# Performance work log

Hardware: AMD Instinct MI355X
Metric: run time of the kernel (lower is better)

The kernel has to match this reference:

```python
import jax, jax.numpy as jnp
import numpy as np

FP8_MAX = 448.0  # finfo(float8_e4m3fn).max
BLK = 128        # block_size = [128, 128]


def _quant_dequant_act(x):
    """Dynamic per-token, per-128-block fp8 quantization followed by dequant.
    Matches fp8_act_quant: scale = amax(block)/448, q = fp8(x/scale), deq = q*scale."""
    T, K = x.shape
    xb = x.reshape(T, K // BLK, BLK)
    amax = jnp.max(jnp.abs(xb), axis=-1, keepdims=True)
    scale = jnp.maximum(amax, 1e-12) / FP8_MAX  # [T, K//BLK, 1]
    q = (xb / scale).astype(jnp.float8_e4m3fn).astype(jnp.float32)
    return (q * scale).reshape(T, K)


def _dequant_weight(w, s):
    """Block-wise dequant of an fp8-valued [N, K] weight with [N//BLK, K//BLK] scales."""
    N, K = w.shape
    wb = w.reshape(N // BLK, BLK, K // BLK, BLK)
    return (wb * s[:, None, :, None]).reshape(N, K)


def setup_inputs() -> dict:
    key = jax.random.key(0)
    ks = jax.random.split(key, 7)
    T, H, I, E, TOPK = 8192, 2048, 1024, 32, 8
    f8 = lambda x: x.astype(jnp.float8_e4m3fn).astype(jnp.float32)  # store fp8-valued weights as f32
    hidden_states = jax.random.normal(ks[0], (T, H), jnp.float32)
    gate_up_proj = f8(jax.random.normal(ks[1], (E, 2 * I, H), jnp.float32))
    gate_up_proj_scale_inv = jax.random.uniform(ks[2], (E, (2 * I) // BLK, H // BLK), jnp.float32, 0.005, 0.02)
    down_proj = f8(jax.random.normal(ks[3], (E, H, I), jnp.float32))
    down_proj_scale_inv = jax.random.uniform(ks[4], (E, H // BLK, I // BLK), jnp.float32, 0.005, 0.02)
    top_k_index = jax.random.randint(ks[5], (T, TOPK), 0, E, jnp.int32)
    tw = jax.random.uniform(ks[6], (T, TOPK), jnp.float32)
    top_k_weights = tw / jnp.sum(tw, axis=-1, keepdims=True)
    return {
        'hidden_states': hidden_states,
        'gate_up_proj': gate_up_proj,
        'gate_up_proj_scale_inv': gate_up_proj_scale_inv,
        'down_proj': down_proj,
        'down_proj_scale_inv': down_proj_scale_inv,
        'top_k_weights': top_k_weights,
        'top_k_index': top_k_index,
    }


def reference(hidden_states, gate_up_proj, gate_up_proj_scale_inv, down_proj,
              down_proj_scale_inv, top_k_weights, top_k_index):
    E = gate_up_proj.shape[0]
    # Dynamic activation quantization is per-token (expert-independent): do it once.
    x_deq = _quant_dequant_act(hidden_states)  # [T, H]
    # Per-expert combine weight: cw[e, t] = sum_k top_k_weights[t,k] * (top_k_index[t,k]==e)
    hit = top_k_index[None, :, :] == jnp.arange(E, dtype=top_k_index.dtype)[:, None, None]
    cw = jnp.sum(jnp.where(hit, top_k_weights[None, :, :], 0.0), axis=-1)  # [E, T]

    def body(acc, xs):
        wgu, sgu, wd, sd, w_tok = xs
        h = x_deq @ _dequant_weight(wgu, sgu).T          # [T, 2I] fp8 grouped GEMM
        gate, up = jnp.split(h, 2, axis=-1)
        h = jax.nn.silu(gate) * up                        # _apply_gate
        h = _quant_dequant_act(h)                         # re-quantize before down_proj
        y = h @ _dequant_weight(wd, sd).T                 # [T, H]
        return acc + w_tok[:, None] * y, None

    acc0 = jnp.zeros_like(hidden_states, dtype=jnp.float32)
    out, _ = jax.lax.scan(
        body, acc0,
        (gate_up_proj, gate_up_proj_scale_inv, down_proj, down_proj_scale_inv, cw))
    return out
```

## Files before the change

kernel.cpp:

```cpp
#include <hip/hip_runtime.h>

typedef float f32x4 __attribute__((ext_vector_type(4)));
typedef float f32x16 __attribute__((ext_vector_type(16)));
typedef _Float16 f16x4 __attribute__((ext_vector_type(4)));
typedef long long i64t;

constexpr int T = 8192, H = 2048, II = 1024, E = 32, TOPK = 8;
constexpr int NSLOT = T * TOPK;
constexpr int MT_MAX = 32;
constexpr int MT1 = 64;

__device__ __forceinline__ i64t frag8(const unsigned char* lds, int row, int kbyte) {
  int c8 = (kbyte >> 3) ^ ((row & 7) << 1) ^ ((row >> 3) & 1);
  return *(const i64t*)(lds + row * 128 + c8 * 8);
}
__device__ __forceinline__ void wr16c(unsigned char* lds, int r, int c, uint4 v) {
  if ((r >> 3) & 1) v = make_uint4(v.z, v.w, v.x, v.y);
  *(uint4*)(lds + r * 128 + ((c ^ (r & 7)) << 4)) = v;
}

__global__ void k_quant_x(const float* __restrict__ x, unsigned char* __restrict__ x8,
                          float* __restrict__ xs) {
  int gw = blockIdx.x * 4 + (threadIdx.x >> 6);
  int lane = threadIdx.x & 63;
  int token = gw >> 4, kb = gw & 15;
  float2 v = *(const float2*)(x + (size_t)token * H + kb * 128 + lane * 2);
  float am = fmaxf(fabsf(v.x), fabsf(v.y));
#pragma unroll
  for (int m = 1; m <= 32; m <<= 1) am = fmaxf(am, __shfl_xor(am, m, 64));
  float scale = fmaxf(am, 1e-12f) / 448.0f;
  int pk = __builtin_amdgcn_cvt_pk_fp8_f32(v.x / scale, v.y / scale, 0, false);
  *(unsigned short*)(x8 + (size_t)token * H + kb * 128 + lane * 2) = (unsigned short)(pk & 0xffff);
  if (lane == 0) xs[token * 16 + kb] = scale;
}

__global__ void k_cvt_w(const float* __restrict__ w, unsigned char* __restrict__ w8, int n4) {
  int i = blockIdx.x * 256 + threadIdx.x;
  if (i >= n4) return;
  f32x4 v = *(const f32x4*)(w + (size_t)i * 4);
  int p = __builtin_amdgcn_cvt_pk_fp8_f32(v[0], v[1], 0, false);
  p = __builtin_amdgcn_cvt_pk_fp8_f32(v[2], v[3], p, true);
  *(unsigned int*)(w8 + (size_t)i * 4) = (unsigned int)p;
}

__global__ void k_count(const int* __restrict__ tki, int* __restrict__ counts) {
  int i = blockIdx.x * 256 + threadIdx.x;
  if (i < NSLOT) atomicAdd(&counts[tki[i]], 1);
}
__global__ void k_scan(const int* __restrict__ counts, int* __restrict__ offsets) {
  if (threadIdx.x == 0) {
    int s = 0;
    for (int e = 0; e < E; ++e) { offsets[e] = s; s += counts[e]; }
    offsets[E] = s;
  }
}
__global__ void k_fill(const int* __restrict__ tki, const float* __restrict__ tkw,
                       const int* __restrict__ offsets, int* __restrict__ cursor,
                       int* __restrict__ tok_list, float* __restrict__ cw_list,
                       int* __restrict__ islot) {
  int i = blockIdx.x * 256 + threadIdx.x;
  if (i < NSLOT) {
    int e = tki[i];
    int pos = atomicAdd(&cursor[e], 1);
    int slot = offsets[e] + pos;
    tok_list[slot] = i >> 3;
    cw_list[slot] = tkw[i];
    islot[i] = slot;
  }
}

__launch_bounds__(256, 2)
__global__ void k_gemm1(const unsigned char* __restrict__ x8, const float* __restrict__ xs,
                        const unsigned char* __restrict__ wgu8, const float* __restrict__ sgu,
                        const int* __restrict__ offsets, const int* __restrict__ tok_list,
                        unsigned char* __restrict__ a8, float* __restrict__ ascale) {
  __shared__ __align__(16) unsigned char lA[64 * 128];
  __shared__ __align__(16) unsigned char lBg[128 * 128];
  __shared__ __align__(16) unsigned char lBu[128 * 128];
  __shared__ float lsx[16 * 64];
  __shared__ int ltok[64];
  __shared__ float lamax[64 * 2];
  __shared__ float lscale[64];

  int bx = blockIdx.x;
  int e = bx >> 9, mt = (bx >> 3) & 63, nt = bx & 7;
  int off0 = offsets[e];
  int Me = offsets[e + 1] - off0;
  if (mt * 64 >= Me) return;
  int vrows = Me - mt * 64; if (vrows > 64) vrows = 64;
  int tid = threadIdx.x;

  if (tid < 64) ltok[tid] = (tid < vrows) ? tok_list[off0 + mt * 64 + tid] : -1;
  __syncthreads();

  if (tid < 128) {
    int r = tid >> 1, h = tid & 1;
    int tokr = ltok[r]; int tk = tokr < 0 ? 0 : tokr;
#pragma unroll
    for (int i = 0; i < 2; ++i) {
      f32x4 v = *(const f32x4*)(xs + (size_t)tk * 16 + h * 8 + i * 4);
#pragma unroll
      for (int j = 0; j < 4; ++j) lsx[(h * 8 + i * 4 + j) * 64 + r] = (tokr < 0) ? 0.0f : v[j];
    }
  }

  const int lane = tid & 63, wid = tid >> 6;
  const int wm = wid >> 1, wn = wid & 1;
  const int l31 = lane & 31, lg = lane >> 5;

  const int ra = tid >> 2, qa = tid & 3;
  const int rb = tid >> 1, hb = tid & 1;
  int tokA = ltok[ra] < 0 ? 0 : ltok[ra];
  const unsigned char* gA = x8 + (size_t)tokA * H + qa * 32;
  const unsigned char* gG = wgu8 + ((size_t)e * 2048 + nt * 128 + rb) * H + hb * 64;
  const unsigned char* gU = gG + (size_t)1024 * H;

  {
    uint4 a0 = *(const uint4*)gA, a1 = *(const uint4*)(gA + 16);
    uint4 g0 = *(const uint4*)gG, g1 = *(const uint4*)(gG + 16);
    uint4 g2 = *(const uint4*)(gG + 32), g3 = *(const uint4*)(gG + 48);
    uint4 u0 = *(const uint4*)gU, u1 = *(const uint4*)(gU + 16);
    uint4 u2 = *(const uint4*)(gU + 32), u3 = *(const uint4*)(gU + 48);
    wr16c(lA, ra, qa * 2 + 0, a0); wr16c(lA, ra, qa * 2 + 1, a1);
    wr16c(lBg, rb, hb * 4 + 0, g0); wr16c(lBg, rb, hb * 4 + 1, g1);
    wr16c(lBg, rb, hb * 4 + 2, g2); wr16c(lBg, rb, hb * 4 + 3, g3);
    wr16c(lBu, rb, hb * 4 + 0, u0); wr16c(lBu, rb, hb * 4 + 1, u1);
    wr16c(lBu, rb, hb * 4 + 2, u2); wr16c(lBu, rb, hb * 4 + 3, u3);
  }
  __syncthreads();

  f32x16 aG[2] = {};
  f32x16 aU[2] = {};

  for (int kb = 0; kb < 16; ++kb) {
    uint4 pA0, pA1, pG0, pG1, pG2, pG3, pU0, pU1, pU2, pU3;
    if (kb < 15) {
      pA0 = *(const uint4*)(gA + (kb + 1) * 128);
      pA1 = *(const uint4*)(gA + (kb + 1) * 128 + 16);
      pG0 = *(const uint4*)(gG + (kb + 1) * 128);
      pG1 = *(const uint4*)(gG + (kb + 1) * 128 + 16);
      pG2 = *(const uint4*)(gG + (kb + 1) * 128 + 32);
      pG3 = *(const uint4*)(gG + (kb + 1) * 128 + 48);
      pU0 = *(const uint4*)(gU + (kb + 1) * 128);
      pU1 = *(const uint4*)(gU + (kb + 1) * 128 + 16);
      pU2 = *(const uint4*)(gU + (kb + 1) * 128 + 32);
      pU3 = *(const uint4*)(gU + (kb + 1) * 128 + 48);
    }

    float swg = sgu[(e * 16 + nt) * 16 + kb];
    float swu = sgu[(e * 16 + 8 + nt) * 16 + kb];

    i64t af[8];
#pragma unroll
    for (int ks = 0; ks < 8; ++ks)
      af[ks] = frag8(lA, wm * 32 + l31, ks * 16 + lg * 8);
    f32x4 sxv[4];
#pragma unroll
    for (int jj = 0; jj < 4; ++jj)
      sxv[jj] = *(const f32x4*)(&lsx[kb * 64 + wm * 32 + jj * 8 + lg * 4]);

#pragma unroll
    for (int gu = 0; gu < 2; ++gu) {
      const unsigned char* lB = gu ? lBu : lBg;
      float sw = gu ? swu : swg;
#pragma unroll
      for (int nf = 0; nf < 2; ++nf) {
        i64t bf[8];
#pragma unroll
        for (int ks = 0; ks < 8; ++ks)
          bf[ks] = frag8(lB, wn * 64 + nf * 32 + l31, ks * 16 + lg * 8);
        f32x16 t = {};
#pragma unroll
        for (int ks = 0; ks < 8; ++ks)
          t = __builtin_amdgcn_mfma_f32_32x32x16_fp8_fp8(af[ks], bf[ks], t, 0, 0, 0);
#pragma unroll
        for (int j = 0; j < 16; ++j) {
          float f = sxv[j >> 2][j & 3] * sw;
          if (gu) aU[nf][j] += t[j] * f; else aG[nf][j] += t[j] * f;
        }
      }
    }

    if (kb < 15) {
      __syncthreads();
      wr16c(lA, ra, qa * 2 + 0, pA0); wr16c(lA, ra, qa * 2 + 1, pA1);
      wr16c(lBg, rb, hb * 4 + 0, pG0); wr16c(lBg, rb, hb * 4 + 1, pG1);
      wr16c(lBg, rb, hb * 4 + 2, pG2); wr16c(lBg, rb, hb * 4 + 3, pG3);
      wr16c(lBu, rb, hb * 4 + 0, pU0); wr16c(lBu, rb, hb * 4 + 1, pU1);
      wr16c(lBu, rb, hb * 4 + 2, pU2); wr16c(lBu, rb, hb * 4 + 3, pU3);
      __syncthreads();
    }
  }

#pragma unroll
  for (int nf = 0; nf < 2; ++nf)
#pragma unroll
    for (int j = 0; j < 16; ++j) {
      float g = aG[nf][j], u = aU[nf][j];
      aG[nf][j] = g * (1.0f / (1.0f + expf(-g))) * u;
    }

#pragma unroll
  for (int j = 0; j < 16; ++j) {
    float m = fmaxf(fabsf(aG[0][j]), fabsf(aG[1][j]));
#pragma unroll
    for (int msk = 1; msk <= 16; msk <<= 1) m = fmaxf(m, __shfl_xor(m, msk, 64));
    if (l31 == 0)
      lamax[(wm * 32 + (j & 3) + ((j >> 2) * 8) + lg * 4) * 2 + wn] = m;
  }
  __syncthreads();
  if (tid < 64) {
    float mm = fmaxf(lamax[tid * 2], lamax[tid * 2 + 1]);
    lscale[tid] = fmaxf(mm, 1e-12f) / 448.0f;
  }
  __syncthreads();

#pragma unroll
  for (int j = 0; j < 16; ++j) {
    int row = wm * 32 + (j & 3) + ((j >> 2) * 8) + lg * 4;
    float sc = lscale[row];
#pragma unroll
    for (int nf = 0; nf < 2; ++nf) {
      int pk = __builtin_amdgcn_cvt_pk_fp8_f32(aG[nf][j] / sc, 0.0f, 0, false);
      lA[row * 128 + wn * 64 + nf * 32 + l31] = (unsigned char)(pk & 0xff);
    }
    if (row < vrows && l31 == 0 && wn == 0)
      ascale[(off0 + mt * 64 + row) * 8 + nt] = sc;
  }
  __syncthreads();
#pragma unroll
  for (int it = 0; it < 2; ++it) {
    int idx = it * 256 + tid;
    int row = idx >> 3, c = idx & 7;
    if (row < vrows)
      *(uint4*)(a8 + (size_t)(off0 + mt * 64 + row) * 1024 + nt * 128 + c * 16) =
          *(const uint4*)(lA + row * 128 + c * 16);
  }
}

__launch_bounds__(256, 2)
__global__ void k_gemm2(const unsigned char* __restrict__ a8, const float* __restrict__ ascale,
                        const unsigned char* __restrict__ wd8, const float* __restrict__ sd,
                        const int* __restrict__ offsets, const float* __restrict__ cw_list,
                        int ntbase, _Float16* __restrict__ yslot) {
  __shared__ __align__(16) unsigned char lbuf[2][2][128 * 128];
  __shared__ float las[8 * 128];
  __shared__ float lcw[128];

  int bx = blockIdx.x;
  int e = bx >> 8, mt = (bx >> 3) & 31, nth = bx & 7;
  int nt = ntbase + nth;
  int off0 = offsets[e];
  int Me = offsets[e + 1] - off0;
  if (mt * 128 >= Me) return;
  int vrows = Me - mt * 128; if (vrows > 128) vrows = 128;
  int tid = threadIdx.x;

  if (tid < 128) lcw[tid] = (tid < vrows) ? cw_list[off0 + mt * 128 + tid] : 0.0f;
  int r = tid >> 1, h = tid & 1;
  int srow = off0 + mt * 128 + r; if (srow > NSLOT - 1) srow = NSLOT - 1;
  {
    f32x4 v = *(const f32x4*)(ascale + (size_t)srow * 8 + h * 4);
#pragma unroll
    for (int j = 0; j < 4; ++j) las[(h * 4 + j) * 128 + r] = v[j];
  }

  const int lane = tid & 63, wid = tid >> 6;
  const int wm = wid >> 1, wn = wid & 1;
  const int l31 = lane & 31, lg = lane >> 5;

  const unsigned char* gA = a8 + (size_t)srow * 1024 + h * 64;
  const unsigned char* gB = wd8 + ((size_t)e * 2048 + nt * 128 + r) * 1024 + h * 64;

  uint4 rA[4], rB[4];
#pragma unroll
  for (int i = 0; i < 4; ++i) { rA[i] = ((const uint4*)gA)[i]; rB[i] = ((const uint4*)gB)[i]; }
#pragma unroll
  for (int i = 0; i < 4; ++i) { wr16c(lbuf[0][0], r, h * 4 + i, rA[i]); wr16c(lbuf[0][1], r, h * 4 + i, rB[i]); }
  __syncthreads();

  f32x16 acc[2][2] = {};
  int cur = 0;

  for (int kb = 0; kb < 8; ++kb) {
    if (kb < 7) {
#pragma unroll
      for (int i = 0; i < 4; ++i) {
        rA[i] = ((const uint4*)(gA + (kb + 1) * 128))[i];
        rB[i] = ((const uint4*)(gB + (kb + 1) * 128))[i];
      }
    }
    const unsigned char* cA = lbuf[cur][0];
    const unsigned char* cB = lbuf[cur][1];
    float swd = sd[(e * 16 + nt) * 8 + kb];
    i64t bf[2][8];
#pragma unroll
    for (int nf = 0; nf < 2; ++nf)
#pragma unroll
      for (int ks = 0; ks < 8; ++ks)
        bf[nf][ks] = frag8(cB, wn * 64 + nf * 32 + l31, ks * 16 + lg * 8);
#pragma unroll
    for (int mf = 0; mf < 2; ++mf) {
      i64t af[8];
#pragma unroll
      for (int ks = 0; ks < 8; ++ks)
        af[ks] = frag8(cA, wm * 64 + mf * 32 + l31, ks * 16 + lg * 8);
      f32x4 sav[4];
#pragma unroll
      for (int jj = 0; jj < 4; ++jj)
        sav[jj] = *(const f32x4*)(&las[kb * 128 + wm * 64 + mf * 32 + jj * 8 + lg * 4]);
#pragma unroll
      for (int nf = 0; nf < 2; ++nf) {
        f32x16 t = {};
#pragma unroll
        for (int ks = 0; ks < 8; ++ks)
          t = __builtin_amdgcn_mfma_f32_32x32x16_fp8_fp8(af[ks], bf[nf][ks], t, 0, 0, 0);
#pragma unroll
        for (int j = 0; j < 16; ++j)
          acc[mf][nf][j] += t[j] * (sav[j >> 2][j & 3] * swd);
      }
    }
    if (kb < 7) {
      unsigned char* nA = lbuf[cur ^ 1][0];
      unsigned char* nB = lbuf[cur ^ 1][1];
#pragma unroll
      for (int i = 0; i < 4; ++i) { wr16c(nA, r, h * 4 + i, rA[i]); wr16c(nB, r, h * 4 + i, rB[i]); }
      __syncthreads();
      cur ^= 1;
    }
  }

  __syncthreads();
  _Float16* lh = (_Float16*)lbuf;
#pragma unroll
  for (int mf = 0; mf < 2; ++mf)
#pragma unroll
    for (int j = 0; j < 16; ++j) {
      int row = wm * 64 + mf * 32 + (j & 3) + ((j >> 2) * 8) + lg * 4;
      float w = lcw[row];
#pragma unroll
      for (int nf = 0; nf < 2; ++nf)
        lh[row * 128 + wn * 64 + nf * 32 + l31] = (_Float16)(acc[mf][nf][j] * w);
    }
  __syncthreads();
#pragma unroll
  for (int it = 0; it < 8; ++it) {
    int idx = it * 256 + tid;
    int row = idx >> 4, u = idx & 15;
    if (row < vrows)
      *(uint4*)((char*)yslot + ((size_t)(off0 + mt * 128 + row) * 1024 + nth * 128) * 2 + u * 16) =
          *(const uint4*)((const char*)lh + row * 256 + u * 16);
  }
}

__global__ void k_reduce(const _Float16* __restrict__ yslot, const int* __restrict__ islot,
                         float* __restrict__ out, int half) {
  __shared__ int ls[8];
  int t = blockIdx.x;
  if (threadIdx.x < 8) ls[threadIdx.x] = islot[t * 8 + threadIdx.x];
  __syncthreads();
  int c = threadIdx.x * 4;
  float s0 = 0, s1 = 0, s2 = 0, s3 = 0;
#pragma unroll
  for (int k = 0; k < 8; ++k) {
    f16x4 v = *(const f16x4*)(yslot + (size_t)ls[k] * 1024 + c);
    s0 += (float)v[0]; s1 += (float)v[1]; s2 += (float)v[2]; s3 += (float)v[3];
  }
  f32x4 r = {s0, s1, s2, s3};
  *(f32x4*)(out + (size_t)t * 2048 + half * 1024 + c) = r;
}

extern "C" void kernel_launch(void* const* d_in, const int* in_sizes, int n_in,
                              void* d_out, int out_size, void* d_ws, size_t ws_size,
                              hipStream_t stream) {
  const float* x   = (const float*)d_in[0];
  const float* wgu = (const float*)d_in[1];
  const float* sgu = (const float*)d_in[2];
  const float* wd  = (const float*)d_in[3];
  const float* sd  = (const float*)d_in[4];
  const float* tkw = (const float*)d_in[5];
  const int*   tki = (const int*)d_in[6];
  float* out = (float*)d_out;

  char* ws = (char*)d_ws;
  size_t o = 0;
  auto alloc = [&](size_t sz) { void* p = ws + o; o = (o + sz + 255) & ~(size_t)255; return p; };
  unsigned char* x8    = (unsigned char*)alloc((size_t)T * H);
  unsigned char* wgu8  = (unsigned char*)alloc((size_t)E * 2 * II * H);
  unsigned char* wd8   = (unsigned char*)alloc((size_t)E * H * II);
  unsigned char* a8    = (unsigned char*)alloc((size_t)NSLOT * II);
  float* xs            = (float*)alloc((size_t)T * 16 * 4);
  float* as_           = (float*)alloc((size_t)NSLOT * 8 * 4);
  int* counts          = (int*)alloc(128);
  int* cursor          = (int*)alloc(128);
  int* offsets         = (int*)alloc(256);
  int* tok_list        = (int*)alloc((size_t)NSLOT * 4);
  float* cw_list       = (float*)alloc((size_t)NSLOT * 4);
  int* islot           = (int*)alloc((size_t)NSLOT * 4);
  _Float16* yslot      = (_Float16*)wgu8;

  hipMemsetAsync(counts, 0, 128, stream);
  hipMemsetAsync(cursor, 0, 128, stream);

  k_quant_x<<<dim3((T * 16) / 4), dim3(256), 0, stream>>>(x, x8, xs);
  k_cvt_w<<<dim3((E * 2 * II * H / 4) / 256), dim3(256), 0, stream>>>(wgu, wgu8, E * 2 * II * H / 4);
  k_cvt_w<<<dim3((E * H * II / 4) / 256), dim3(256), 0, stream>>>(wd, wd8, E * H * II / 4);
  k_count<<<dim3(NSLOT / 256), dim3(256), 0, stream>>>(tki, counts);
  k_scan<<<dim3(1), dim3(64), 0, stream>>>(counts, offsets);
  k_fill<<<dim3(NSLOT / 256), dim3(256), 0, stream>>>(tki, tkw, offsets, cursor, tok_list, cw_list, islot);
  k_gemm1<<<dim3(E * MT1 * 8), dim3(256), 0, stream>>>(x8, xs, wgu8, sgu, offsets, tok_list, a8, as_);
  k_gemm2<<<dim3(E * MT_MAX * 8), dim3(256), 0, stream>>>(a8, as_, wd8, sd, offsets, cw_list, 0, yslot);
  k_reduce<<<dim3(T), dim3(256), 0, stream>>>(yslot, islot, out, 0);
  k_gemm2<<<dim3(E * MT_MAX * 8), dim3(256), 0, stream>>>(a8, as_, wd8, sd, offsets, cw_list, 8, yslot);
  k_reduce<<<dim3(T), dim3(256), 0, stream>>>(yslot, islot, out, 1);
}
```

Baseline: 1.586 ms.

## Pre-swizzle fp8 weights and stream GEMM operands via direct global-to-LDS loads

```diff
diff --git a/kernel.cpp b/kernel.cpp
--- a/kernel.cpp
+++ b/kernel.cpp
@@ -7,8 +7,14 @@
 
 constexpr int T = 8192, H = 2048, II = 1024, E = 32, TOPK = 8;
 constexpr int NSLOT = T * TOPK;
+constexpr int NSLOT_P = NSLOT + E * 16 + 128;
 constexpr int MT_MAX = 32;
 constexpr int MT1 = 64;
+
+__device__ __forceinline__ void gload16(const unsigned char* g, unsigned char* l) {
+  __builtin_amdgcn_global_load_lds((const __attribute__((address_space(1))) unsigned int*)g,
+                                   (__attribute__((address_space(3))) unsigned int*)l, 16, 0, 0);
+}
 
 __device__ __forceinline__ i64t frag8(const unsigned char* lds, int row, int kbyte) {
   int c8 = (kbyte >> 3) ^ ((row & 7) << 1) ^ ((row >> 3) & 1);
@@ -34,13 +40,26 @@
   if (lane == 0) xs[token * 16 + kb] = scale;
 }
 
-__global__ void k_cvt_w(const float* __restrict__ w, unsigned char* __restrict__ w8, int n4) {
+__global__ void k_cvt_w_sw(const float* __restrict__ w, unsigned char* __restrict__ w8,
+                           int cpr , int nchunk) {
   int i = blockIdx.x * 256 + threadIdx.x;
-  if (i >= n4) return;
-  f32x4 v = *(const f32x4*)(w + (size_t)i * 4);
-  int p = __builtin_amdgcn_cvt_pk_fp8_f32(v[0], v[1], 0, false);
-  p = __builtin_amdgcn_cvt_pk_fp8_f32(v[2], v[3], p, true);
-  *(unsigned int*)(w8 + (size_t)i * 4) = (unsigned int)p;
+  if (i >= nchunk) return;
+  int row = i / cpr;
+  int within = i - row * cpr;
+  int kb = within >> 3, pc = within & 7;
+  int lc = pc ^ (row & 7);
+  int sw = ((row >> 3) & 1) ? 8 : 0;
+  const float* src = w + (size_t)row * ((size_t)cpr * 16) + kb * 128 + lc * 16;
+  unsigned int o[4];
+#pragma unroll
+  for (int k = 0; k < 4; ++k) {
+    int e0 = (4 * k + sw) & 15;
+    f32x4 v = *(const f32x4*)(src + e0);
+    int p = __builtin_amdgcn_cvt_pk_fp8_f32(v[0], v[1], 0, false);
+    p = __builtin_amdgcn_cvt_pk_fp8_f32(v[2], v[3], p, true);
+    o[k] = (unsigned int)p;
+  }
+  *(uint4*)(w8 + (size_t)i * 16) = make_uint4(o[0], o[1], o[2], o[3]);
 }
 
 __global__ void k_count(const int* __restrict__ tki, int* __restrict__ counts) {
@@ -50,7 +69,7 @@
 __global__ void k_scan(const int* __restrict__ counts, int* __restrict__ offsets) {
   if (threadIdx.x == 0) {
     int s = 0;
-    for (int e = 0; e < E; ++e) { offsets[e] = s; s += counts[e]; }
+    for (int e = 0; e < E; ++e) { offsets[e] = s; s += ((counts[e] + 15) >> 4) << 4; }
     offsets[E] = s;
   }
 }
@@ -72,11 +91,12 @@
 __launch_bounds__(256, 2)
 __global__ void k_gemm1(const unsigned char* __restrict__ x8, const float* __restrict__ xs,
                         const unsigned char* __restrict__ wgu8, const float* __restrict__ sgu,
-                        const int* __restrict__ offsets, const int* __restrict__ tok_list,
+                        const int* __restrict__ offsets, const int* __restrict__ counts,
+                        const int* __restrict__ tok_list,
                         unsigned char* __restrict__ a8, float* __restrict__ ascale) {
   __shared__ __align__(16) unsigned char lA[64 * 128];
-  __shared__ __align__(16) unsigned char lBg[128 * 128];
-  __shared__ __align__(16) unsigned char lBu[128 * 128];
+  __shared__ __align__(16) unsigned char lBg[2][128 * 128];
+  __shared__ __align__(16) unsigned char lBu[2][128 * 128];
   __shared__ float lsx[16 * 64];
   __shared__ int ltok[64];
   __shared__ float lamax[64 * 2];
@@ -85,7 +105,7 @@
   int bx = blockIdx.x;
   int e = bx >> 9, mt = (bx >> 3) & 63, nt = bx & 7;
   int off0 = offsets[e];
-  int Me = offsets[e + 1] - off0;
+  int Me = counts[e];
   if (mt * 64 >= Me) return;
   int vrows = Me - mt * 64; if (vrows > 64) vrows = 64;
   int tid = threadIdx.x;
@@ -109,42 +129,44 @@
   const int l31 = lane & 31, lg = lane >> 5;
 
   const int ra = tid >> 2, qa = tid & 3;
-  const int rb = tid >> 1, hb = tid & 1;
   int tokA = ltok[ra] < 0 ? 0 : ltok[ra];
   const unsigned char* gA = x8 + (size_t)tokA * H + qa * 32;
-  const unsigned char* gG = wgu8 + ((size_t)e * 2048 + nt * 128 + rb) * H + hb * 64;
-  const unsigned char* gU = gG + (size_t)1024 * H;
+
+  const int lr = lane >> 3, lc8 = lane & 7;
+  const unsigned char* pG[4];
+  const unsigned char* pU[4];
+#pragma unroll
+  for (int i = 0; i < 4; ++i) {
+    int row = wid * 32 + i * 8 + lr;
+    pG[i] = wgu8 + ((size_t)e * 2048 + nt * 128 + row) * H + lc8 * 16;
+    pU[i] = pG[i] + (size_t)1024 * H;
+  }
 
   {
     uint4 a0 = *(const uint4*)gA, a1 = *(const uint4*)(gA + 16);
-    uint4 g0 = *(const uint4*)gG, g1 = *(const uint4*)(gG + 16);
-    uint4 g2 = *(const uint4*)(gG + 32), g3 = *(const uint4*)(gG + 48);
-    uint4 u0 = *(const uint4*)gU, u1 = *(const uint4*)(gU + 16);
-    uint4 u2 = *(const uint4*)(gU + 32), u3 = *(const uint4*)(gU + 48);
     wr16c(lA, ra, qa * 2 + 0, a0); wr16c(lA, ra, qa * 2 + 1, a1);
-    wr16c(lBg, rb, hb * 4 + 0, g0); wr16c(lBg, rb, hb * 4 + 1, g1);
-    wr16c(lBg, rb, hb * 4 + 2, g2); wr16c(lBg, rb, hb * 4 + 3, g3);
-    wr16c(lBu, rb, hb * 4 + 0, u0); wr16c(lBu, rb, hb * 4 + 1, u1);
-    wr16c(lBu, rb, hb * 4 + 2, u2); wr16c(lBu, rb, hb * 4 + 3, u3);
+  }
+#pragma unroll
+  for (int i = 0; i < 4; ++i) {
+    gload16(pG[i], lBg[0] + wid * 4096 + i * 1024);
+    gload16(pU[i], lBu[0] + wid * 4096 + i * 1024);
   }
   __syncthreads();
 
   f32x16 aG[2] = {};
   f32x16 aU[2] = {};
+  int cur = 0;
 
   for (int kb = 0; kb < 16; ++kb) {
-    uint4 pA0, pA1, pG0, pG1, pG2, pG3, pU0, pU1, pU2, pU3;
+    uint4 pA0, pA1;
     if (kb < 15) {
+#pragma unroll
+      for (int i = 0; i < 4; ++i) {
+        gload16(pG[i] + (kb + 1) * 128, lBg[cur ^ 1] + wid * 4096 + i * 1024);
+        gload16(pU[i] + (kb + 1) * 128, lBu[cur ^ 1] + wid * 4096 + i * 1024);
+      }
       pA0 = *(const uint4*)(gA + (kb + 1) * 128);
       pA1 = *(const uint4*)(gA + (kb + 1) * 128 + 16);
-      pG0 = *(const uint4*)(gG + (kb + 1) * 128);
-      pG1 = *(const uint4*)(gG + (kb + 1) * 128 + 16);
-      pG2 = *(const uint4*)(gG + (kb + 1) * 128 + 32);
-      pG3 = *(const uint4*)(gG + (kb + 1) * 128 + 48);
-      pU0 = *(const uint4*)(gU + (kb + 1) * 128);
-      pU1 = *(const uint4*)(gU + (kb + 1) * 128 + 16);
-      pU2 = *(const uint4*)(gU + (kb + 1) * 128 + 32);
-      pU3 = *(const uint4*)(gU + (kb + 1) * 128 + 48);
     }
 
     float swg = sgu[(e * 16 + nt) * 16 + kb];
@@ -161,7 +183,7 @@
 
 #pragma unroll
     for (int gu = 0; gu < 2; ++gu) {
-      const unsigned char* lB = gu ? lBu : lBg;
+      const unsigned char* lB = gu ? lBu[cur] : lBg[cur];
       float sw = gu ? swu : swg;
 #pragma unroll
       for (int nf = 0; nf < 2; ++nf) {
@@ -184,11 +206,8 @@
     if (kb < 15) {
       __syncthreads();
       wr16c(lA, ra, qa * 2 + 0, pA0); wr16c(lA, ra, qa * 2 + 1, pA1);
-      wr16c(lBg, rb, hb * 4 + 0, pG0); wr16c(lBg, rb, hb * 4 + 1, pG1);
-      wr16c(lBg, rb, hb * 4 + 2, pG2); wr16c(lBg, rb, hb * 4 + 3, pG3);
-      wr16c(lBu, rb, hb * 4 + 0, pU0); wr16c(lBu, rb, hb * 4 + 1, pU1);
-      wr16c(lBu, rb, hb * 4 + 2, pU2); wr16c(lBu, rb, hb * 4 + 3, pU3);
       __syncthreads();
+      cur ^= 1;
     }
   }
 
@@ -219,10 +238,12 @@
   for (int j = 0; j < 16; ++j) {
     int row = wm * 32 + (j & 3) + ((j >> 2) * 8) + lg * 4;
     float sc = lscale[row];
+    int hs = ((row >> 3) & 1) ? 8 : 0;
 #pragma unroll
     for (int nf = 0; nf < 2; ++nf) {
+      int col = wn * 64 + nf * 32 + l31;
       int pk = __builtin_amdgcn_cvt_pk_fp8_f32(aG[nf][j] / sc, 0.0f, 0, false);
-      lA[row * 128 + wn * 64 + nf * 32 + l31] = (unsigned char)(pk & 0xff);
+      lA[row * 128 + (((col >> 4) ^ (row & 7)) << 4) + ((col & 15) ^ hs)] = (unsigned char)(pk & 0xff);
     }
     if (row < vrows && l31 == 0 && wn == 0)
       ascale[(off0 + mt * 64 + row) * 8 + nt] = sc;
@@ -241,7 +262,8 @@
 __launch_bounds__(256, 2)
 __global__ void k_gemm2(const unsigned char* __restrict__ a8, const float* __restrict__ ascale,
                         const unsigned char* __restrict__ wd8, const float* __restrict__ sd,
-                        const int* __restrict__ offsets, const float* __restrict__ cw_list,
+                        const int* __restrict__ offsets, const int* __restrict__ counts,
+                        const float* __restrict__ cw_list,
                         int ntbase, _Float16* __restrict__ yslot) {
   __shared__ __align__(16) unsigned char lbuf[2][2][128 * 128];
   __shared__ float las[8 * 128];
@@ -251,15 +273,16 @@
   int e = bx >> 8, mt = (bx >> 3) & 31, nth = bx & 7;
   int nt = ntbase + nth;
   int off0 = offsets[e];
-  int Me = offsets[e + 1] - off0;
+  int Me = counts[e];
   if (mt * 128 >= Me) return;
   int vrows = Me - mt * 128; if (vrows > 128) vrows = 128;
   int tid = threadIdx.x;
-
-  if (tid < 128) lcw[tid] = (tid < vrows) ? cw_list[off0 + mt * 128 + tid] : 0.0f;
-  int r = tid >> 1, h = tid & 1;
-  int srow = off0 + mt * 128 + r; if (srow > NSLOT - 1) srow = NSLOT - 1;
+  const int rowbase = off0 + mt * 128;
+
+  if (tid < 128) lcw[tid] = (tid < vrows) ? cw_list[rowbase + tid] : 0.0f;
   {
+    int r = tid >> 1, h = tid & 1;
+    int srow = rowbase + r; if (srow > NSLOT_P - 1) srow = NSLOT_P - 1;
     f32x4 v = *(const f32x4*)(ascale + (size_t)srow * 8 + h * 4);
 #pragma unroll
     for (int j = 0; j < 4; ++j) las[(h * 4 + j) * 128 + r] = v[j];
@@ -269,14 +292,21 @@
   const int wm = wid >> 1, wn = wid & 1;
   const int l31 = lane & 31, lg = lane >> 5;
 
-  const unsigned char* gA = a8 + (size_t)srow * 1024 + h * 64;
-  const unsigned char* gB = wd8 + ((size_t)e * 2048 + nt * 128 + r) * 1024 + h * 64;
-
-  uint4 rA[4], rB[4];
-#pragma unroll
-  for (int i = 0; i < 4; ++i) { rA[i] = ((const uint4*)gA)[i]; rB[i] = ((const uint4*)gB)[i]; }
-#pragma unroll
-  for (int i = 0; i < 4; ++i) { wr16c(lbuf[0][0], r, h * 4 + i, rA[i]); wr16c(lbuf[0][1], r, h * 4 + i, rB[i]); }
+  const int lr = lane >> 3, lc8 = lane & 7;
+  const unsigned char* pA[4];
+  const unsigned char* pB[4];
+#pragma unroll
+  for (int i = 0; i < 4; ++i) {
+    int row = wid * 32 + i * 8 + lr;
+    pA[i] = a8 + (size_t)(rowbase + row) * 1024 + lc8 * 16;
+    pB[i] = wd8 + ((size_t)e * 2048 + nt * 128 + row) * 1024 + lc8 * 16;
+  }
+
+#pragma unroll
+  for (int i = 0; i < 4; ++i) {
+    gload16(pA[i], lbuf[0][0] + wid * 4096 + i * 1024);
+    gload16(pB[i], lbuf[0][1] + wid * 4096 + i * 1024);
+  }
   __syncthreads();
 
   f32x16 acc[2][2] = {};
@@ -286,8 +316,8 @@
     if (kb < 7) {
 #pragma unroll
       for (int i = 0; i < 4; ++i) {
-        rA[i] = ((const uint4*)(gA + (kb + 1) * 128))[i];
-        rB[i] = ((const uint4*)(gB + (kb + 1) * 128))[i];
+        gload16(pA[i] + (kb + 1) * 128, lbuf[cur ^ 1][0] + wid * 4096 + i * 1024);
+        gload16(pB[i] + (kb + 1) * 128, lbuf[cur ^ 1][1] + wid * 4096 + i * 1024);
       }
     }
     const unsigned char* cA = lbuf[cur][0];
@@ -320,17 +350,10 @@
           acc[mf][nf][j] += t[j] * (sav[j >> 2][j & 3] * swd);
       }
     }
-    if (kb < 7) {
-      unsigned char* nA = lbuf[cur ^ 1][0];
-      unsigned char* nB = lbuf[cur ^ 1][1];
-#pragma unroll
-      for (int i = 0; i < 4; ++i) { wr16c(nA, r, h * 4 + i, rA[i]); wr16c(nB, r, h * 4 + i, rB[i]); }
-      __syncthreads();
-      cur ^= 1;
-    }
-  }
-
-  __syncthreads();
+    __syncthreads();
+    cur ^= 1;
+  }
+
   _Float16* lh = (_Float16*)lbuf;
 #pragma unroll
   for (int mf = 0; mf < 2; ++mf)
@@ -348,7 +371,7 @@
     int idx = it * 256 + tid;
     int row = idx >> 4, u = idx & 15;
     if (row < vrows)
-      *(uint4*)((char*)yslot + ((size_t)(off0 + mt * 128 + row) * 1024 + nth * 128) * 2 + u * 16) =
+      *(uint4*)((char*)yslot + ((size_t)(rowbase + row) * 1024 + nth * 128) * 2 + u * 16) =
           *(const uint4*)((const char*)lh + row * 256 + u * 16);
   }
 }
@@ -385,17 +408,19 @@
   char* ws = (char*)d_ws;
   size_t o = 0;
   auto alloc = [&](size_t sz) { void* p = ws + o; o = (o + sz + 255) & ~(size_t)255; return p; };
+  size_t wgu_sz = (size_t)E * 2 * II * H;
+  size_t ysl_sz = (size_t)NSLOT_P * II * 2;
   unsigned char* x8    = (unsigned char*)alloc((size_t)T * H);
-  unsigned char* wgu8  = (unsigned char*)alloc((size_t)E * 2 * II * H);
+  unsigned char* wgu8  = (unsigned char*)alloc(wgu_sz > ysl_sz ? wgu_sz : ysl_sz);
   unsigned char* wd8   = (unsigned char*)alloc((size_t)E * H * II);
-  unsigned char* a8    = (unsigned char*)alloc((size_t)NSLOT * II);
+  unsigned char* a8    = (unsigned char*)alloc((size_t)NSLOT_P * II);
   float* xs            = (float*)alloc((size_t)T * 16 * 4);
-  float* as_           = (float*)alloc((size_t)NSLOT * 8 * 4);
+  float* as_           = (float*)alloc((size_t)NSLOT_P * 8 * 4);
   int* counts          = (int*)alloc(128);
   int* cursor          = (int*)alloc(128);
   int* offsets         = (int*)alloc(256);
-  int* tok_list        = (int*)alloc((size_t)NSLOT * 4);
-  float* cw_list       = (float*)alloc((size_t)NSLOT * 4);
+  int* tok_list        = (int*)alloc((size_t)NSLOT_P * 4);
+  float* cw_list       = (float*)alloc((size_t)NSLOT_P * 4);
   int* islot           = (int*)alloc((size_t)NSLOT * 4);
   _Float16* yslot      = (_Float16*)wgu8;
 
@@ -403,14 +428,14 @@
   hipMemsetAsync(cursor, 0, 128, stream);
 
   k_quant_x<<<dim3((T * 16) / 4), dim3(256), 0, stream>>>(x, x8, xs);
-  k_cvt_w<<<dim3((E * 2 * II * H / 4) / 256), dim3(256), 0, stream>>>(wgu, wgu8, E * 2 * II * H / 4);
-  k_cvt_w<<<dim3((E * H * II / 4) / 256), dim3(256), 0, stream>>>(wd, wd8, E * H * II / 4);
+  k_cvt_w_sw<<<dim3((E * 2 * II * H / 16) / 256), dim3(256), 0, stream>>>(wgu, wgu8, H / 16, E * 2 * II * H / 16);
+  k_cvt_w_sw<<<dim3((E * H * II / 16) / 256), dim3(256), 0, stream>>>(wd, wd8, II / 16, E * H * II / 16);
   k_count<<<dim3(NSLOT / 256), dim3(256), 0, stream>>>(tki, counts);
   k_scan<<<dim3(1), dim3(64), 0, stream>>>(counts, offsets);
   k_fill<<<dim3(NSLOT / 256), dim3(256), 0, stream>>>(tki, tkw, offsets, cursor, tok_list, cw_list, islot);
-  k_gemm1<<<dim3(E * MT1 * 8), dim3(256), 0, stream>>>(x8, xs, wgu8, sgu, offsets, tok_list, a8, as_);
-  k_gemm2<<<dim3(E * MT_MAX * 8), dim3(256), 0, stream>>>(a8, as_, wd8, sd, offsets, cw_list, 0, yslot);
+  k_gemm1<<<dim3(E * MT1 * 8), dim3(256), 0, stream>>>(x8, xs, wgu8, sgu, offsets, counts, tok_list, a8, as_);
+  k_gemm2<<<dim3(E * MT_MAX * 8), dim3(256), 0, stream>>>(a8, as_, wd8, sd, offsets, counts, cw_list, 0, yslot);
   k_reduce<<<dim3(T), dim3(256), 0, stream>>>(yslot, islot, out, 0);
-  k_gemm2<<<dim3(E * MT_MAX * 8), dim3(256), 0, stream>>>(a8, as_, wd8, sd, offsets, cw_list, 8, yslot);
+  k_gemm2<<<dim3(E * MT_MAX * 8), dim3(256), 0, stream>>>(a8, as_, wd8, sd, offsets, counts, cw_list, 8, yslot);
   k_reduce<<<dim3(T), dim3(256), 0, stream>>>(yslot, islot, out, 1);
 }
```

Measured after the change: 1.569 ms (median of 2 runs). No clear change (-1.1%).
